# Kernel tuning notes

Hardware: AMD Instinct MI355X
Metric: run time of the kernel (lower is better)

## Reference

```python
import jax, jax.numpy as jnp
import numpy as np

DM, NEXPERTS, SETS, ESIZE = 1024, 32, 4, 32
B, S = 2, 8192


def setup_inputs() -> dict:
    key = jax.random.key(0)
    ks = jax.random.split(key, 7)
    sc = 0.02
    return {
        "x": jax.random.normal(ks[0], (B, S, DM), jnp.float32),
        "Wc": jax.random.normal(ks[1], (DM, NEXPERTS, SETS), jnp.float32) * sc,
        "bc": jax.random.normal(ks[2], (NEXPERTS, SETS), jnp.float32) * sc,
        "W1": jax.random.normal(ks[3], (NEXPERTS, SETS, DM, ESIZE), jnp.float32) * sc,
        "b1": jax.random.normal(ks[4], (NEXPERTS, SETS, ESIZE), jnp.float32) * sc,
        "W2": jax.random.normal(ks[5], (NEXPERTS, SETS, DM, ESIZE), jnp.float32) * sc,
        "b2": jax.random.normal(ks[6], (NEXPERTS, SETS, DM), jnp.float32) * sc,
    }


def reference(x, Wc, bc, W1, b1, W2, b2):
    b, s, d = x.shape
    g = Wc.shape[1]          # nexperts (= tokens per group)
    # group tokens: [..., (n g), d] -> [..., n, g, d]
    grouped = x.reshape(b, s // g, g, d)
    # controller logits: [b, n, t, e, s]
    logits = jnp.einsum('bntd,des->bntes', grouped, Wc) + bc
    # tie-breaker varying along the token axis (dim -3)
    tie = jnp.linspace(0.0, 1e-6, g, dtype=x.dtype).reshape(-1, 1, 1)
    logits = logits + tie
    # hard one-hot permutation: argmax over tokens per (expert, set)
    perm = (logits == jnp.max(logits, axis=-3, keepdims=True)).astype(x.dtype)
    # dispatch: [b, n, e, s, d]
    permuted = jnp.einsum('bntd,bntes->bnesd', grouped, perm)
    # per-(expert,set) MLP
    inner = jax.nn.relu(jnp.einsum('bnesd,esdf->bnesf', permuted, W1) + b1)
    result_permuted = jnp.einsum('bnesf,esdf->bnesd', inner, W2) + b2
    # combine back to tokens: [b, n, t, d]
    result = jnp.einsum('bnesd,bntes->bntd', result_permuted, perm)
    return result.reshape(b, s, d)
```

## Files before the change

### kernel.cpp

```cpp
#include <hip/hip_runtime.h>
#include <hip/hip_bf16.h>

#define DM   1024
#define NES  128
#define GT   32
#define NGRP 512
#define FSZ  32

typedef float f32x4 __attribute__((ext_vector_type(4)));
typedef short s16x8 __attribute__((ext_vector_type(8)));

__device__ inline unsigned short f2bf(float f) {
  union { float f; unsigned int u; } x; x.f = f;
  unsigned int r = x.u + 0x7fffu + ((x.u >> 16) & 1u);
  return (unsigned short)(r >> 16);
}
__device__ inline float bf2f(unsigned short h) {
  union { unsigned int u; float f; } x; x.u = ((unsigned int)h) << 16;
  return x.f;
}

__global__ __launch_bounds__(256, 2) void kA(const float* __restrict__ x,
                                             const float* __restrict__ Wc,
                                             const float* __restrict__ bc,
                                             unsigned int* __restrict__ sel,
                                             unsigned short* __restrict__ xb) {
  __shared__ float wcs[64 * 128];
  __shared__ float xs[32 * 64];
  __shared__ float lg[32 * 128];
  const int g   = blockIdx.x;
  const int tid = threadIdx.x;
  const int es0 = (tid & 31) * 4;
  const int t0  = (tid >> 5) * 4;
  const float* xg = x + (size_t)g * GT * DM;

  float acc[16];
#pragma unroll
  for (int i = 0; i < 16; ++i) acc[i] = 0.f;

  for (int c = 0; c < 16; ++c) {
    const int d0 = c * 64;
    if (c) __syncthreads();
#pragma unroll
    for (int k = 0; k < 8; ++k) {
      int idx = (tid + 256 * k) * 4;
      int dd = idx >> 7, es = idx & 127;
      *(float4*)&wcs[idx] = *(const float4*)&Wc[(size_t)(d0 + dd) * NES + es];
    }
#pragma unroll
    for (int k = 0; k < 2; ++k) {
      int idx = (tid + 256 * k) * 4;
      int t = idx >> 6, dd = idx & 63;
      *(float4*)&xs[idx] = *(const float4*)&xg[(size_t)t * DM + d0 + dd];
    }
    __syncthreads();

    {
      int idx = tid * 8;
      int t = idx >> 6, col = idx & 63;
      float4 a = *(const float4*)&xs[idx];
      float4 b = *(const float4*)&xs[idx + 4];
      s16x8 v;
      v[0] = (short)f2bf(a.x); v[1] = (short)f2bf(a.y);
      v[2] = (short)f2bf(a.z); v[3] = (short)f2bf(a.w);
      v[4] = (short)f2bf(b.x); v[5] = (short)f2bf(b.y);
      v[6] = (short)f2bf(b.z); v[7] = (short)f2bf(b.w);
      *(s16x8*)&xb[((size_t)g * GT + t) * DM + d0 + col] = v;
    }

    float part[16];
#pragma unroll
    for (int i = 0; i < 16; ++i) part[i] = 0.f;
#pragma unroll 4
    for (int dd = 0; dd < 64; dd += 4) {
      float4 w0 = *(const float4*)&wcs[(dd + 0) * NES + es0];
      float4 w1 = *(const float4*)&wcs[(dd + 1) * NES + es0];
      float4 w2 = *(const float4*)&wcs[(dd + 2) * NES + es0];
      float4 w3 = *(const float4*)&wcs[(dd + 3) * NES + es0];
      float4 xv0 = *(const float4*)&xs[(t0 + 0) * 64 + dd];
      float4 xv1 = *(const float4*)&xs[(t0 + 1) * 64 + dd];
      float4 xv2 = *(const float4*)&xs[(t0 + 2) * 64 + dd];
      float4 xv3 = *(const float4*)&xs[(t0 + 3) * 64 + dd];
#define KSTEP(i, XV)                                                       \
      part[i*4+0] = fmaf(XV.x, w0.x, part[i*4+0]);                         \
      part[i*4+1] = fmaf(XV.x, w0.y, part[i*4+1]);                         \
      part[i*4+2] = fmaf(XV.x, w0.z, part[i*4+2]);                         \
      part[i*4+3] = fmaf(XV.x, w0.w, part[i*4+3]);                         \
      part[i*4+0] = fmaf(XV.y, w1.x, part[i*4+0]);                         \
      part[i*4+1] = fmaf(XV.y, w1.y, part[i*4+1]);                         \
      part[i*4+2] = fmaf(XV.y, w1.z, part[i*4+2]);                         \
      part[i*4+3] = fmaf(XV.y, w1.w, part[i*4+3]);                         \
      part[i*4+0] = fmaf(XV.z, w2.x, part[i*4+0]);                         \
      part[i*4+1] = fmaf(XV.z, w2.y, part[i*4+1]);                         \
      part[i*4+2] = fmaf(XV.z, w2.z, part[i*4+2]);                         \
      part[i*4+3] = fmaf(XV.z, w2.w, part[i*4+3]);                         \
      part[i*4+0] = fmaf(XV.w, w3.x, part[i*4+0]);                         \
      part[i*4+1] = fmaf(XV.w, w3.y, part[i*4+1]);                         \
      part[i*4+2] = fmaf(XV.w, w3.z, part[i*4+2]);                         \
      part[i*4+3] = fmaf(XV.w, w3.w, part[i*4+3]);
      KSTEP(0, xv0) KSTEP(1, xv1) KSTEP(2, xv2) KSTEP(3, xv3)
#undef KSTEP
    }
#pragma unroll
    for (int i = 0; i < 16; ++i) acc[i] += part[i];
  }
  __syncthreads();

#pragma unroll
  for (int i = 0; i < 4; ++i) {
    int t = t0 + i;
    float tie = (float)((double)t * (1e-6 / 31.0));
#pragma unroll
    for (int j = 0; j < 4; ++j) {
      int es = es0 + j;
      lg[t * NES + es] = (acc[i * 4 + j] + bc[es]) + tie;
    }
  }
  __syncthreads();
  if (tid < NES) {
    float m = -INFINITY;
    for (int t = 0; t < GT; ++t) m = fmaxf(m, lg[t * NES + tid]);
    unsigned int msk = 0u;
    for (int t = 0; t < GT; ++t) if (lg[t * NES + tid] == m) msk |= (1u << t);
    sel[(size_t)g * NES + tid] = msk;
  }
}

__global__ __launch_bounds__(256) void kW2(const float* __restrict__ W2,
                                           unsigned short* __restrict__ W2f) {
  int idx = blockIdx.x * 256 + threadIdx.x;
  int l = idx & 63, dt = (idx >> 6) & 63, es = idx >> 12;
  const float* src = W2 + ((size_t)es * DM + dt * 16 + (l & 15)) * FSZ + (l >> 4) * 8;
  float4 a = *(const float4*)src;
  float4 b = *(const float4*)(src + 4);
  s16x8 v;
  v[0] = (short)f2bf(a.x); v[1] = (short)f2bf(a.y);
  v[2] = (short)f2bf(a.z); v[3] = (short)f2bf(a.w);
  v[4] = (short)f2bf(b.x); v[5] = (short)f2bf(b.y);
  v[6] = (short)f2bf(b.z); v[7] = (short)f2bf(b.w);
  *(s16x8*)(W2f + (size_t)idx * 8) = v;
}

__global__ __launch_bounds__(256) void kW1(const float* __restrict__ W1,
                                           unsigned short* __restrict__ W1f) {
  int idx = blockIdx.x * 256 + threadIdx.x;
  int l = idx & 63, nh = (idx >> 6) & 1, kt = (idx >> 7) & 31, es = idx >> 12;
  const float* src = W1 + ((size_t)es * DM + kt * 32 + (l >> 4) * 8) * FSZ
                        + nh * 16 + (l & 15);
  s16x8 v;
#pragma unroll
  for (int i = 0; i < 8; ++i) v[i] = (short)f2bf(src[(size_t)i * FSZ]);
  *(s16x8*)(W1f + (size_t)idx * 8) = v;
}

__global__ __launch_bounds__(256, 2) void kBm(const unsigned short* __restrict__ xb,
                                              const unsigned short* __restrict__ W1f,
                                              const float* __restrict__ b1,
                                              const unsigned int* __restrict__ sel,
                                              unsigned short* __restrict__ innerb) {
  __shared__ unsigned short As[128 * 128];
  __shared__ int tokL[128];
  __shared__ unsigned int mulL[128];
  const int bid = blockIdx.x;
  const int es = bid >> 2, g0 = (bid & 3) * 128;
  const int tid = threadIdx.x;
  const int l = tid & 63, w = tid >> 6;
  const int r15 = l & 15, q = l >> 4;
  const int mw = w * 32;

  if (tid < 128) {
    unsigned int m = sel[(size_t)(g0 + tid) * NES + es];
    tokL[tid] = (g0 + tid) * GT + (__ffs(m) - 1);
    mulL[tid] = (m & (m - 1)) ? m : 0u;
  }

  const int r = tid >> 1, p = tid & 1;
  const int swz = (r & 7) << 4;
  const unsigned int dbase = (unsigned int)r * 256 + (unsigned int)p * 128;

  f32x4 acc[2][2];
#pragma unroll
  for (int i = 0; i < 2; ++i)
#pragma unroll
    for (int j = 0; j < 2; ++j) acc[i][j] = (f32x4){0.f, 0.f, 0.f, 0.f};

  for (int c = 0; c < 8; ++c) {
    __syncthreads();
    unsigned int mm = mulL[r];
    if (!mm) {
      const unsigned short* src = xb + (size_t)tokL[r] * DM + c * 128 + p * 64;
#pragma unroll
      for (int j = 0; j < 8; ++j) {
        s16x8 v = *(const s16x8*)(src + j * 8);
        *(s16x8*)((char*)As + ((dbase + j * 16) ^ swz)) = v;
      }
    } else {
      size_t grow = (size_t)(g0 + r) * GT;
#pragma unroll
      for (int j = 0; j < 8; ++j) {
        float av[8] = {0.f, 0.f, 0.f, 0.f, 0.f, 0.f, 0.f, 0.f};
        unsigned int m2 = mm;
        while (m2) {
          int tt = __ffs(m2) - 1; m2 &= m2 - 1;
          s16x8 v = *(const s16x8*)(xb + (grow + tt) * DM + c * 128 + p * 64 + j * 8);
#pragma unroll
          for (int k = 0; k < 8; ++k) av[k] += bf2f((unsigned short)v[k]);
        }
        s16x8 o;
#pragma unroll
        for (int k = 0; k < 8; ++k) o[k] = (short)f2bf(av[k]);
        *(s16x8*)((char*)As + ((dbase + j * 16) ^ swz)) = o;
      }
    }
    __syncthreads();

#pragma unroll
    for (int s = 0; s < 4; ++s) {
      const int ks = c * 4 + s;
      const unsigned short* bp = W1f + ((size_t)es * 32 + ks) * 1024 + l * 8;
      s16x8 bf0 = *(const s16x8*)bp;
      s16x8 bf1 = *(const s16x8*)(bp + 512);
      const int row0 = mw + r15, row1 = mw + 16 + r15;
      s16x8 a0 = *(const s16x8*)((char*)As +
                   (((unsigned)row0 * 256 + s * 64 + q * 16) ^ ((row0 & 7) << 4)));
      s16x8 a1 = *(const s16x8*)((char*)As +
                   (((unsigned)row1 * 256 + s * 64 + q * 16) ^ ((row1 & 7) << 4)));
      acc[0][0] = __builtin_amdgcn_mfma_f32_16x16x32_bf16(a0, bf0, acc[0][0], 0, 0, 0);
      acc[0][1] = __builtin_amdgcn_mfma_f32_16x16x32_bf16(a0, bf1, acc[0][1], 0, 0, 0);
      acc[1][0] = __builtin_amdgcn_mfma_f32_16x16x32_bf16(a1, bf0, acc[1][0], 0, 0, 0);
      acc[1][1] = __builtin_amdgcn_mfma_f32_16x16x32_bf16(a1, bf1, acc[1][1], 0, 0, 0);
    }
  }

  float bia0 = b1[es * FSZ + r15];
  float bia1 = b1[es * FSZ + 16 + r15];
#pragma unroll
  for (int i = 0; i < 2; ++i)
#pragma unroll
    for (int rr = 0; rr < 4; ++rr) {
      int g = g0 + mw + i * 16 + q * 4 + rr;
      unsigned short* op = innerb + ((size_t)es * NGRP + g) * FSZ;
      op[r15]      = f2bf(fmaxf(acc[i][0][rr] + bia0, 0.f));
      op[16 + r15] = f2bf(fmaxf(acc[i][1][rr] + bia1, 0.f));
    }
}

__global__ __launch_bounds__(256) void kC1(const unsigned short* __restrict__ innerb,
                                           const unsigned short* __restrict__ W2f,
                                           const float* __restrict__ b2,
                                           unsigned short* __restrict__ Rb,
                                           int es0, int Ec) {
  const int bid = blockIdx.x;
  const int esl = bid >> 5;
  const int es  = es0 + esl;
  const int mt  = (bid >> 3) & 3;
  const int nt  = bid & 7;
  const int tid = threadIdx.x;
  const int l = tid & 63, w = tid >> 6;
  const int r15 = l & 15, q = l >> 4;
  const int g0 = mt * 128 + (w >> 1) * 64;
  const int n0 = nt * 128 + (w & 1) * 64;

  const unsigned short* Ab = innerb + ((size_t)es * NGRP + g0 + r15) * FSZ + q * 8;
  const unsigned short* Bb = W2f + (((size_t)es * 64 + (n0 >> 4)) * 64 + l) * 8;
  s16x8 a[4], b[4];
#pragma unroll
  for (int i = 0; i < 4; ++i) a[i] = *(const s16x8*)(Ab + (size_t)i * 16 * FSZ);
#pragma unroll
  for (int j = 0; j < 4; ++j) b[j] = *(const s16x8*)(Bb + (size_t)j * 64 * 8);

  const f32x4 z = {0.f, 0.f, 0.f, 0.f};
  f32x4 acc[4][4];
#pragma unroll
  for (int i = 0; i < 4; ++i)
#pragma unroll
    for (int j = 0; j < 4; ++j)
      acc[i][j] = __builtin_amdgcn_mfma_f32_16x16x32_bf16(a[i], b[j], z, 0, 0, 0);

#pragma unroll
  for (int j = 0; j < 4; ++j) {
    const int col = n0 + j * 16 + r15;
    const float b2v = b2[(size_t)es * DM + col];
#pragma unroll
    for (int i = 0; i < 4; ++i) {
#pragma unroll
      for (int r = 0; r < 4; ++r) {
        const int g = g0 + i * 16 + q * 4 + r;
        Rb[((size_t)g * Ec + esl) * DM + col] = f2bf(acc[i][j][r] + b2v);
      }
    }
  }
}

__global__ __launch_bounds__(256) void kC2(const unsigned short* __restrict__ Rb,
                                           const unsigned int* __restrict__ sel,
                                           float* __restrict__ out,
                                           int es0, int Ec, int direct) {
  __shared__ unsigned int cnt[32];
  __shared__ unsigned char list[32][128];
  const int bid = blockIdx.x;
  const int g = bid >> 2, dq = bid & 3;
  const int tid = threadIdx.x;
  if (tid < 32) cnt[tid] = 0;
  __syncthreads();
  if (tid < Ec) {
    unsigned int m = sel[(size_t)g * NES + es0 + tid];
    while (m) { int t = __ffs(m) - 1; m &= m - 1;
      unsigned int p = atomicAdd(&cnt[t], 1u);
      list[t][p] = (unsigned char)tid; }
  }
  __syncthreads();
  const int t = tid >> 3, part = tid & 7;
  const int d0 = dq * 256 + part * 32;
  const int n = (int)cnt[t];
  const unsigned short* base = Rb + (size_t)g * Ec * DM + d0;

  float acc[32];
#pragma unroll
  for (int i = 0; i < 32; ++i) acc[i] = 0.f;

  s16x8 cur[4];
  if (n) {
    const unsigned short* r = base + (size_t)list[t][0] * DM;
#pragma unroll
    for (int v = 0; v < 4; ++v) cur[v] = *(const s16x8*)(r + v * 8);
  }
  for (int e = 0; e < n; ++e) {
    s16x8 nxt[4];
    const bool more = (e + 1 < n);
    if (more) {
      const unsigned short* r = base + (size_t)list[t][e + 1] * DM;
#pragma unroll
      for (int v = 0; v < 4; ++v) nxt[v] = *(const s16x8*)(r + v * 8);
    }
#pragma unroll
    for (int v = 0; v < 4; ++v)
#pragma unroll
      for (int k = 0; k < 8; ++k)
        acc[v * 8 + k] += bf2f((unsigned short)cur[v][k]);
    if (more) {
#pragma unroll
      for (int v = 0; v < 4; ++v) cur[v] = nxt[v];
    }
  }

  float* op = out + ((size_t)g * GT + t) * DM + d0;
  if (direct) {
#pragma unroll
    for (int v = 0; v < 8; ++v)
      *(float4*)&op[v * 4] =
          make_float4(acc[v * 4], acc[v * 4 + 1], acc[v * 4 + 2], acc[v * 4 + 3]);
  } else {
#pragma unroll
    for (int v = 0; v < 8; ++v) {
      float4 o = *(float4*)&op[v * 4];
      o.x += acc[v * 4]; o.y += acc[v * 4 + 1];
      o.z += acc[v * 4 + 2]; o.w += acc[v * 4 + 3];
      *(float4*)&op[v * 4] = o;
    }
  }
}

extern "C" void kernel_launch(void* const* d_in, const int* in_sizes, int n_in,
                              void* d_out, int out_size, void* d_ws, size_t ws_size,
                              hipStream_t stream) {
  const float* x  = (const float*)d_in[0];
  const float* Wc = (const float*)d_in[1];
  const float* bc = (const float*)d_in[2];
  const float* W1 = (const float*)d_in[3];
  const float* b1 = (const float*)d_in[4];
  const float* W2 = (const float*)d_in[5];
  const float* b2 = (const float*)d_in[6];
  float* out = (float*)d_out;

  unsigned int* sel = (unsigned int*)d_ws;
  unsigned short* innerb = (unsigned short*)((char*)d_ws + (1u << 20));
  unsigned short* W2f = (unsigned short*)((char*)d_ws + (6u << 20));
  unsigned short* W1f = (unsigned short*)((char*)d_ws + (15u << 20));
  unsigned short* xb  = (unsigned short*)((char*)d_ws + (24u << 20));
  unsigned short* Rb  = (unsigned short*)((char*)d_ws + (15u << 20));

  int Ec = 128;
  while (Ec > 1 && (15u << 20) + (size_t)NGRP * Ec * DM * 2 > ws_size) Ec >>= 1;
  const int NC = NES / Ec;

  if (NC > 1)
    hipMemsetAsync(d_out, 0, (size_t)out_size * sizeof(float), stream);
  kA<<<NGRP, 256, 0, stream>>>(x, Wc, bc, sel, xb);
  kW2<<<2048, 256, 0, stream>>>(W2, W2f);
  kW1<<<2048, 256, 0, stream>>>(W1, W1f);
  kBm<<<NGRP, 256, 0, stream>>>(xb, W1f, b1, sel, innerb);
  for (int c = 0; c < NC; ++c) {
    kC1<<<Ec * 32, 256, 0, stream>>>(innerb, W2f, b2, Rb, c * Ec, Ec);
    kC2<<<NGRP * 4, 256, 0, stream>>>(Rb, sel, out, c * Ec, Ec, NC == 1);
  }
}
```

Measured before the change: 211.4 us.

## Double-buffer controller kernel with direct global-to-LDS loads and merge weight-conversion kernels

Reworks the controller-logit kernel so each 32-wide K chunk of Wc and x is loaded straight into LDS with global_load_lds into one of two buffers, prefetching the next chunk while the current one is computed. This is meant to hide global load latency that the old load-then-sync loop exposed, and it reuses the buffer memory for the logits stage to keep LDS usage down. Separately, the W1 and W2 bf16 conversion kernels are merged into one launch to cut launch overhead. The waitcnt plus barrier at the end of each iteration still serialises somewhat, and smaller chunks mean twice as many barriers.

```diff
diff --git a/kernel.cpp b/kernel.cpp
--- a/kernel.cpp
+++ b/kernel.cpp
@@ -10,6 +10,10 @@
 typedef float f32x4 __attribute__((ext_vector_type(4)));
 typedef short s16x8 __attribute__((ext_vector_type(8)));
 
+#define GL2LDS(gp, lp) __builtin_amdgcn_global_load_lds(                      \
+    (const __attribute__((address_space(1))) void*)(gp),                     \
+    (__attribute__((address_space(3))) void*)(lp), 16, 0, 0)
+
 __device__ inline unsigned short f2bf(float f) {
   union { float f; unsigned int u; } x; x.f = f;
   unsigned int r = x.u + 0x7fffu + ((x.u >> 16) & 1u);
@@ -25,62 +29,68 @@
                                              const float* __restrict__ bc,
                                              unsigned int* __restrict__ sel,
                                              unsigned short* __restrict__ xb) {
-  __shared__ float wcs[64 * 128];
-  __shared__ float xs[32 * 64];
-  __shared__ float lg[32 * 128];
+  __shared__ float smem[10240];
+  float* const wcsA = smem;
+  float* const wcsB = smem + 4096;
+  float* const xsA  = smem + 8192;
+  float* const xsB  = smem + 9216;
+  float* const lg   = smem;
   const int g   = blockIdx.x;
   const int tid = threadIdx.x;
+  const int l   = tid & 63, w = tid >> 6;
   const int es0 = (tid & 31) * 4;
   const int t0  = (tid >> 5) * 4;
   const float* xg = x + (size_t)g * GT * DM;
 
-  float acc[16];
+  float acc[16], part[16];
 #pragma unroll
   for (int i = 0; i < 16; ++i) acc[i] = 0.f;
 
-  for (int c = 0; c < 16; ++c) {
-    const int d0 = c * 64;
-    if (c) __syncthreads();
-#pragma unroll
-    for (int k = 0; k < 8; ++k) {
-      int idx = (tid + 256 * k) * 4;
-      int dd = idx >> 7, es = idx & 127;
-      *(float4*)&wcs[idx] = *(const float4*)&Wc[(size_t)(d0 + dd) * NES + es];
-    }
-#pragma unroll
-    for (int k = 0; k < 2; ++k) {
-      int idx = (tid + 256 * k) * 4;
-      int t = idx >> 6, dd = idx & 63;
-      *(float4*)&xs[idx] = *(const float4*)&xg[(size_t)t * DM + d0 + dd];
-    }
-    __syncthreads();
+  auto STAGE = [&](int c, float* wdst, float* xdst) {
+    const int d0 = c * 32;
+#pragma unroll
+    for (int kk = 0; kk < 4; ++kk) {
+      int e4 = w * 1024 + kk * 256 + l * 4;
+      GL2LDS(Wc + (size_t)(d0 + (e4 >> 7)) * NES + (e4 & 127),
+             wdst + w * 1024 + kk * 256);
+    }
+    int ex = w * 256 + l * 4;
+    GL2LDS(xg + (size_t)(ex >> 5) * DM + d0 + (ex & 31), xdst + w * 256);
+  };
+
+  STAGE(0, wcsA, xsA);
+  asm volatile("s_waitcnt vmcnt(0)" ::: "memory");
+  __syncthreads();
+
+  for (int c = 0; c < 32; ++c) {
+    const int b = c & 1;
+    const float* wp = b ? wcsB : wcsA;
+    const float* xp = b ? xsB : xsA;
+    if (c < 31) STAGE(c + 1, b ? wcsA : wcsB, b ? xsA : xsB);
 
     {
-      int idx = tid * 8;
-      int t = idx >> 6, col = idx & 63;
-      float4 a = *(const float4*)&xs[idx];
-      float4 b = *(const float4*)&xs[idx + 4];
-      s16x8 v;
-      v[0] = (short)f2bf(a.x); v[1] = (short)f2bf(a.y);
-      v[2] = (short)f2bf(a.z); v[3] = (short)f2bf(a.w);
-      v[4] = (short)f2bf(b.x); v[5] = (short)f2bf(b.y);
-      v[6] = (short)f2bf(b.z); v[7] = (short)f2bf(b.w);
-      *(s16x8*)&xb[((size_t)g * GT + t) * DM + d0 + col] = v;
-    }
-
-    float part[16];
-#pragma unroll
-    for (int i = 0; i < 16; ++i) part[i] = 0.f;
-#pragma unroll 4
-    for (int dd = 0; dd < 64; dd += 4) {
-      float4 w0 = *(const float4*)&wcs[(dd + 0) * NES + es0];
-      float4 w1 = *(const float4*)&wcs[(dd + 1) * NES + es0];
-      float4 w2 = *(const float4*)&wcs[(dd + 2) * NES + es0];
-      float4 w3 = *(const float4*)&wcs[(dd + 3) * NES + es0];
-      float4 xv0 = *(const float4*)&xs[(t0 + 0) * 64 + dd];
-      float4 xv1 = *(const float4*)&xs[(t0 + 1) * 64 + dd];
-      float4 xv2 = *(const float4*)&xs[(t0 + 2) * 64 + dd];
-      float4 xv3 = *(const float4*)&xs[(t0 + 3) * 64 + dd];
+      int idx = tid * 4;
+      float4 a4 = *(const float4*)&xp[idx];
+      short4 v;
+      v.x = (short)f2bf(a4.x); v.y = (short)f2bf(a4.y);
+      v.z = (short)f2bf(a4.z); v.w = (short)f2bf(a4.w);
+      *(short4*)&xb[((size_t)g * GT + (idx >> 5)) * DM + c * 32 + (idx & 31)] = v;
+    }
+
+    if ((c & 1) == 0) {
+#pragma unroll
+      for (int i = 0; i < 16; ++i) part[i] = 0.f;
+    }
+#pragma unroll 2
+    for (int dd = 0; dd < 32; dd += 4) {
+      float4 w0 = *(const float4*)&wp[(dd + 0) * NES + es0];
+      float4 w1 = *(const float4*)&wp[(dd + 1) * NES + es0];
+      float4 w2 = *(const float4*)&wp[(dd + 2) * NES + es0];
+      float4 w3 = *(const float4*)&wp[(dd + 3) * NES + es0];
+      float4 xv0 = *(const float4*)&xp[(t0 + 0) * 32 + dd];
+      float4 xv1 = *(const float4*)&xp[(t0 + 1) * 32 + dd];
+      float4 xv2 = *(const float4*)&xp[(t0 + 2) * 32 + dd];
+      float4 xv3 = *(const float4*)&xp[(t0 + 3) * 32 + dd];
 #define KSTEP(i, XV)                                                       \
       part[i*4+0] = fmaf(XV.x, w0.x, part[i*4+0]);                         \
       part[i*4+1] = fmaf(XV.x, w0.y, part[i*4+1]);                         \
@@ -101,10 +111,13 @@
       KSTEP(0, xv0) KSTEP(1, xv1) KSTEP(2, xv2) KSTEP(3, xv3)
 #undef KSTEP
     }
-#pragma unroll
-    for (int i = 0; i < 16; ++i) acc[i] += part[i];
-  }
-  __syncthreads();
+    if (c & 1) {
+#pragma unroll
+      for (int i = 0; i < 16; ++i) acc[i] += part[i];
+    }
+    asm volatile("s_waitcnt vmcnt(0)" ::: "memory");
+    __syncthreads();
+  }
 
 #pragma unroll
   for (int i = 0; i < 4; ++i) {
@@ -126,31 +139,33 @@
   }
 }
 
-__global__ __launch_bounds__(256) void kW2(const float* __restrict__ W2,
-                                           unsigned short* __restrict__ W2f) {
-  int idx = blockIdx.x * 256 + threadIdx.x;
-  int l = idx & 63, dt = (idx >> 6) & 63, es = idx >> 12;
-  const float* src = W2 + ((size_t)es * DM + dt * 16 + (l & 15)) * FSZ + (l >> 4) * 8;
-  float4 a = *(const float4*)src;
-  float4 b = *(const float4*)(src + 4);
-  s16x8 v;
-  v[0] = (short)f2bf(a.x); v[1] = (short)f2bf(a.y);
-  v[2] = (short)f2bf(a.z); v[3] = (short)f2bf(a.w);
-  v[4] = (short)f2bf(b.x); v[5] = (short)f2bf(b.y);
-  v[6] = (short)f2bf(b.z); v[7] = (short)f2bf(b.w);
-  *(s16x8*)(W2f + (size_t)idx * 8) = v;
-}
-
-__global__ __launch_bounds__(256) void kW1(const float* __restrict__ W1,
-                                           unsigned short* __restrict__ W1f) {
-  int idx = blockIdx.x * 256 + threadIdx.x;
-  int l = idx & 63, nh = (idx >> 6) & 1, kt = (idx >> 7) & 31, es = idx >> 12;
-  const float* src = W1 + ((size_t)es * DM + kt * 32 + (l >> 4) * 8) * FSZ
-                        + nh * 16 + (l & 15);
-  s16x8 v;
-#pragma unroll
-  for (int i = 0; i < 8; ++i) v[i] = (short)f2bf(src[(size_t)i * FSZ]);
-  *(s16x8*)(W1f + (size_t)idx * 8) = v;
+__global__ __launch_bounds__(256) void kW(const float* __restrict__ W1,
+                                          const float* __restrict__ W2,
+                                          unsigned short* __restrict__ W1f,
+                                          unsigned short* __restrict__ W2f) {
+  const int bid = blockIdx.x;
+  if (bid < 2048) {
+    int idx = bid * 256 + threadIdx.x;
+    int l = idx & 63, nh = (idx >> 6) & 1, kt = (idx >> 7) & 31, es = idx >> 12;
+    const float* src = W1 + ((size_t)es * DM + kt * 32 + (l >> 4) * 8) * FSZ
+                          + nh * 16 + (l & 15);
+    s16x8 v;
+#pragma unroll
+    for (int i = 0; i < 8; ++i) v[i] = (short)f2bf(src[(size_t)i * FSZ]);
+    *(s16x8*)(W1f + (size_t)idx * 8) = v;
+  } else {
+    int idx = (bid - 2048) * 256 + threadIdx.x;
+    int l = idx & 63, dt = (idx >> 6) & 63, es = idx >> 12;
+    const float* src = W2 + ((size_t)es * DM + dt * 16 + (l & 15)) * FSZ + (l >> 4) * 8;
+    float4 a = *(const float4*)src;
+    float4 b = *(const float4*)(src + 4);
+    s16x8 v;
+    v[0] = (short)f2bf(a.x); v[1] = (short)f2bf(a.y);
+    v[2] = (short)f2bf(a.z); v[3] = (short)f2bf(a.w);
+    v[4] = (short)f2bf(b.x); v[5] = (short)f2bf(b.y);
+    v[6] = (short)f2bf(b.z); v[7] = (short)f2bf(b.w);
+    *(s16x8*)(W2f + (size_t)idx * 8) = v;
+  }
 }
 
 __global__ __launch_bounds__(256, 2) void kBm(const unsigned short* __restrict__ xb,
@@ -387,8 +402,7 @@
   if (NC > 1)
     hipMemsetAsync(d_out, 0, (size_t)out_size * sizeof(float), stream);
   kA<<<NGRP, 256, 0, stream>>>(x, Wc, bc, sel, xb);
-  kW2<<<2048, 256, 0, stream>>>(W2, W2f);
-  kW1<<<2048, 256, 0, stream>>>(W1, W1f);
+  kW<<<4096, 256, 0, stream>>>(W1, W2, W1f, W2f);
   kBm<<<NGRP, 256, 0, stream>>>(xb, W1f, b1, sel, innerb);
   for (int c = 0; c < NC; ++c) {
     kC1<<<Ec * 32, 256, 0, stream>>>(innerb, W2f, b2, Rb, c * Ec, Ec);
```

New measurement: 214.3 us. About the same (+1.4%).
